# Performance work log

Measured on AMD Instinct MI355X. Metric: run time of the kernel, lower is better.

The kernel has to match this reference:

```python
import jax, jax.numpy as jnp
import numpy as np

N_NODES = 50000
N_EDGES = 800000
D_IN = 128
D_HID = 128
N_CLASSES = 40


def setup_inputs() -> dict:
    key = jax.random.key(0)
    ks = jax.random.split(key, 12)
    x = jax.random.normal(ks[0], (N_NODES, D_IN), dtype=jnp.float32)
    edge_index = jax.random.randint(ks[1], (2, N_EDGES), 0, N_NODES, dtype=jnp.int64)
    s1 = 1.0 / np.sqrt(D_IN)
    s2 = 1.0 / np.sqrt(D_HID)
    W1 = jax.random.uniform(ks[2], (D_IN, D_HID), jnp.float32, -s1, s1)
    b1 = jnp.zeros((D_HID,), jnp.float32)
    W2 = jax.random.uniform(ks[3], (D_HID, D_HID), jnp.float32, -s2, s2)
    b2 = jnp.zeros((D_HID,), jnp.float32)
    W3 = jax.random.uniform(ks[4], (D_HID, D_HID), jnp.float32, -s2, s2)
    b3 = jnp.zeros((D_HID,), jnp.float32)
    fcW = jax.random.uniform(ks[5], (D_HID, N_CLASSES), jnp.float32, -s2, s2)
    fcb = jax.random.uniform(ks[6], (N_CLASSES,), jnp.float32, -s2, s2)
    return {"x": x, "edge_index": edge_index, "W1": W1, "b1": b1,
            "W2": W2, "b2": b2, "W3": W3, "b3": b3, "fcW": fcW, "fcb": fcb}


def _gcn_norm(edge_index, n_nodes):
    # add self-loops, compute symmetric normalization deg^-1/2[src]*deg^-1/2[dst]
    loops = jnp.arange(n_nodes, dtype=edge_index.dtype)
    src = jnp.concatenate([edge_index[0], loops])
    dst = jnp.concatenate([edge_index[1], loops])
    deg = jax.ops.segment_sum(jnp.ones_like(dst, dtype=jnp.float32), dst,
                              num_segments=n_nodes)
    dinv = jax.lax.rsqrt(deg)  # deg >= 1 thanks to self-loops
    norm = dinv[src] * dinv[dst]  # [E+N]
    return src, dst, norm


def _gcn_conv(h, W, b, src, dst, norm, n_nodes):
    h = h @ W                               # [N, D]
    msg = h[src] * norm[:, None]            # [E+N, D] gather + scale
    out = jax.ops.segment_sum(msg, dst, num_segments=n_nodes)  # scatter-add
    return out + b


def reference(x, edge_index, W1, b1, W2, b2, W3, b3, fcW, fcb):
    n = x.shape[0]
    src, dst, norm = _gcn_norm(edge_index, n)
    h = jax.nn.relu(_gcn_conv(x, W1, b1, src, dst, norm, n))
    h = jax.nn.relu(_gcn_conv(h, W2, b2, src, dst, norm, n))
    h = jax.nn.relu(_gcn_conv(h, W3, b3, src, dst, norm, n))
    out = h @ fcW + fcb
    return (h, out)
```

## Files before the change

kernel.cpp:

```cpp
#include <hip/hip_runtime.h>
#include <hip/hip_fp16.h>

#define NN 50000
#define NE 800000
#define D  128
#define NC 40
#define NBLK ((NN + 255) / 256)
#define NXCD 8
#define DRANGE ((NN + NXCD - 1) / NXCD)
#define EPB 2048
#define NCH ((NE + EPB - 1) / EPB)
#define CAP 64
#define NTILE ((NN + 127) / 128)

typedef short bf16x8 __attribute__((ext_vector_type(8)));
typedef float f32x16 __attribute__((ext_vector_type(16)));

__device__ __forceinline__ void load_edge(const void* ei, int e, int is64, int& s, int& d) {
    if (is64) {
        const long long* p = (const long long*)ei;
        s = (int)p[e]; d = (int)p[NE + e];
    } else {
        const int* p = (const int*)ei;
        s = p[e]; d = p[NE + e];
    }
}

__global__ __launch_bounds__(256) void setup_kernel(int* __restrict__ cnt,
                                                    const int* __restrict__ ei,
                                                    int* __restrict__ flag) {
    if (blockIdx.x == NBLK) {
        __shared__ int nz;
        if (threadIdx.x == 0) nz = 0;
        __syncthreads();
        int c = 0;
        for (int i = threadIdx.x; i < 2048; i += 256)
            if (ei[2 * i + 1] != 0) c = 1;
        if (c) atomicAdd(&nz, 1);
        __syncthreads();
        if (threadIdx.x == 0) *flag = (nz == 0) ? 1 : 0;
    } else {
        int i = blockIdx.x * 256 + threadIdx.x;
        if (i < NN) cnt[i] = 0;
    }
}

__global__ __launch_bounds__(256) void fill_kernel(const void* ei, const int* __restrict__ flag,
                                                   int* cnt, int* __restrict__ srcs) {
    int r = blockIdx.x & (NXCD - 1);
    int chunk = blockIdx.x >> 3;
    int base = chunk * EPB;
    int dlo = r * DRANGE, dhi = dlo + DRANGE;
    int is64 = *flag;
#pragma unroll
    for (int j = 0; j < EPB / 256; ++j) {
        int e = base + threadIdx.x + j * 256;
        if (e >= NE) break;
        int s, d; load_edge(ei, e, is64, s, d);
        if (d < dlo || d >= dhi || (unsigned)d >= NN || (unsigned)s >= NN) continue;
        int slot = atomicAdd(&cnt[d], 1);
        if (slot < CAP) srcs[d * CAP + slot] = s;
    }
}

__global__ __launch_bounds__(256) void dinv_kernel(const int* __restrict__ cnt,
                                                   float* __restrict__ dinv) {
    int i = blockIdx.x * 256 + threadIdx.x;
    if (i < NN) dinv[i] = 1.0f / sqrtf((float)cnt[i] + 1.0f);
}

__global__ __launch_bounds__(256) void sort_kernel(const int* __restrict__ cnt,
                                                   int* __restrict__ srcs,
                                                   float* __restrict__ wts,
                                                   const float* __restrict__ dinv) {
    int wid = (blockIdx.x * 256 + threadIdx.x) >> 6;
    int lane = threadIdx.x & 63;
    if (wid >= NN) return;
    int deg = cnt[wid]; if (deg > CAP) deg = CAP;
    if (deg == 0) return;
    float di = dinv[wid];
    int base = wid * CAP;
    int v = (lane < deg) ? srcs[base + lane] : 0x7fffffff;
#pragma unroll
    for (int k = 2; k <= 64; k <<= 1) {
#pragma unroll
        for (int j = k >> 1; j > 0; j >>= 1) {
            int o = __shfl_xor(v, j);
            bool up = ((lane & k) == 0);
            bool lower = ((lane & j) == 0);
            int mn = min(v, o), mx = max(v, o);
            v = (lower == up) ? mn : mx;
        }
    }
    if (lane < deg) {
        srcs[base + lane] = v;
        wts[base + lane] = dinv[v] * di;
    }
}

__device__ __forceinline__ ushort f2bf(float x) {
    unsigned u = __float_as_uint(x);
    return (ushort)((u + 0x7fffu + ((u >> 16) & 1u)) >> 16);
}
__device__ __forceinline__ float bf2f(ushort h) {
    return __uint_as_float(((unsigned)h) << 16);
}

__global__ __launch_bounds__(128) void prep_all_kernel(const float* __restrict__ W1,
                                                       const float* __restrict__ W2,
                                                       const float* __restrict__ W3,
                                                       const float* __restrict__ fcW,
                                                       ushort* __restrict__ i1,
                                                       ushort* __restrict__ i2,
                                                       ushort* __restrict__ i3,
                                                       ushort* __restrict__ ifc) {
    int b = blockIdx.x;
    int k = threadIdx.x;
    if (b < 384) {
        const float* W = (b < 128) ? W1 : (b < 256) ? W2 : W3;
        ushort* img = (b < 128) ? i1 : (b < 256) ? i2 : i3;
        int c = b & 127;
        float w = W[(size_t)k * D + c];
        ushort hi = f2bf(w);
        ushort lo = f2bf(w - bf2f(hi));
        int ch = k >> 6, kk = k & 63, g = kk >> 3;
        int idx = c * 64 + ((g ^ (c & 7)) * 8) + (kk & 7);
        img[(size_t)(ch * 2 + 0) * 8192 + idx] = hi;
        img[(size_t)(ch * 2 + 1) * 8192 + idx] = lo;
    } else {
        int c = b - 384;
        float w = (c < NC) ? fcW[(size_t)k * NC + c] : 0.0f;
        ushort hi = f2bf(w);
        ushort lo = f2bf(w - bf2f(hi));
        int g = k >> 3;
        int idx = c * 128 + ((g ^ (c & 7)) * 8) + (k & 7);
        ifc[idx] = hi;
        ifc[8192 + idx] = lo;
    }
}

__global__ __launch_bounds__(256, 2) void gemm_f32_kernel(const float* __restrict__ A,
                                                          const ushort* __restrict__ Wimg,
                                                          ushort* __restrict__ T) {
    __shared__ alignas(16) ushort sAh[8192];
    __shared__ alignas(16) ushort sAl[8192];
    __shared__ alignas(16) ushort sWh[8192];
    __shared__ alignas(16) ushort sWl[8192];
    int tid = threadIdx.x;
    int wave = tid >> 6, lane = tid & 63;
    int wr = wave >> 1, wc = wave & 1;
    int m0 = blockIdx.x * 128;
    f32x16 acc[2][2];
#pragma unroll
    for (int i = 0; i < 2; ++i)
#pragma unroll
        for (int j = 0; j < 2; ++j)
#pragma unroll
            for (int q = 0; q < 16; ++q) acc[i][j][q] = 0.0f;

    for (int ch = 0; ch < 2; ++ch) {
        const float4* wh = (const float4*)(Wimg + (size_t)(ch * 2 + 0) * 8192);
        const float4* wl = (const float4*)(Wimg + (size_t)(ch * 2 + 1) * 8192);
#pragma unroll
        for (int i = 0; i < 4; ++i) {
            ((float4*)sWh)[tid + i * 256] = wh[tid + i * 256];
            ((float4*)sWl)[tid + i * 256] = wl[tid + i * 256];
        }
#pragma unroll
        for (int p = 0; p < 8; ++p) {
            int idx = tid + p * 256;
            int r = idx >> 4;
            int kq = idx & 15;
            float4 v = make_float4(0, 0, 0, 0);
            int grow = m0 + r;
            if (grow < NN) v = *(const float4*)(A + (size_t)grow * D + ch * 64 + kq * 4);
            ushort4 h, l;
            h.x = f2bf(v.x); l.x = f2bf(v.x - bf2f(h.x));
            h.y = f2bf(v.y); l.y = f2bf(v.y - bf2f(h.y));
            h.z = f2bf(v.z); l.z = f2bf(v.z - bf2f(h.z));
            h.w = f2bf(v.w); l.w = f2bf(v.w - bf2f(h.w));
            int g = kq >> 1, half = kq & 1;
            int uidx = r * 64 + ((g ^ (r & 7)) * 8) + half * 4;
            *(ushort4*)&sAh[uidx] = h;
            *(ushort4*)&sAl[uidx] = l;
        }
        __syncthreads();

        int rb = wr * 64 + (lane & 31);
        int cb = wc * 64 + (lane & 31);
#pragma unroll
        for (int s = 0; s < 4; ++s) {
            int gg = s * 2 + (lane >> 5);
            int ra0 = rb, ra1 = rb + 32;
            int ca0 = cb, ca1 = cb + 32;
            bf16x8 ah0 = *(const bf16x8*)&sAh[ra0 * 64 + ((gg ^ (ra0 & 7)) * 8)];
            bf16x8 ah1 = *(const bf16x8*)&sAh[ra1 * 64 + ((gg ^ (ra1 & 7)) * 8)];
            bf16x8 al0 = *(const bf16x8*)&sAl[ra0 * 64 + ((gg ^ (ra0 & 7)) * 8)];
            bf16x8 al1 = *(const bf16x8*)&sAl[ra1 * 64 + ((gg ^ (ra1 & 7)) * 8)];
            bf16x8 wh0 = *(const bf16x8*)&sWh[ca0 * 64 + ((gg ^ (ca0 & 7)) * 8)];
            bf16x8 wh1 = *(const bf16x8*)&sWh[ca1 * 64 + ((gg ^ (ca1 & 7)) * 8)];
            bf16x8 wl0 = *(const bf16x8*)&sWl[ca0 * 64 + ((gg ^ (ca0 & 7)) * 8)];
            bf16x8 wl1 = *(const bf16x8*)&sWl[ca1 * 64 + ((gg ^ (ca1 & 7)) * 8)];
            acc[0][0] = __builtin_amdgcn_mfma_f32_32x32x16_bf16(ah0, wh0, acc[0][0], 0, 0, 0);
            acc[0][0] = __builtin_amdgcn_mfma_f32_32x32x16_bf16(ah0, wl0, acc[0][0], 0, 0, 0);
            acc[0][0] = __builtin_amdgcn_mfma_f32_32x32x16_bf16(al0, wh0, acc[0][0], 0, 0, 0);
            acc[0][1] = __builtin_amdgcn_mfma_f32_32x32x16_bf16(ah0, wh1, acc[0][1], 0, 0, 0);
            acc[0][1] = __builtin_amdgcn_mfma_f32_32x32x16_bf16(ah0, wl1, acc[0][1], 0, 0, 0);
            acc[0][1] = __builtin_amdgcn_mfma_f32_32x32x16_bf16(al0, wh1, acc[0][1], 0, 0, 0);
            acc[1][0] = __builtin_amdgcn_mfma_f32_32x32x16_bf16(ah1, wh0, acc[1][0], 0, 0, 0);
            acc[1][0] = __builtin_amdgcn_mfma_f32_32x32x16_bf16(ah1, wl0, acc[1][0], 0, 0, 0);
            acc[1][0] = __builtin_amdgcn_mfma_f32_32x32x16_bf16(al1, wh0, acc[1][0], 0, 0, 0);
            acc[1][1] = __builtin_amdgcn_mfma_f32_32x32x16_bf16(ah1, wh1, acc[1][1], 0, 0, 0);
            acc[1][1] = __builtin_amdgcn_mfma_f32_32x32x16_bf16(ah1, wl1, acc[1][1], 0, 0, 0);
            acc[1][1] = __builtin_amdgcn_mfma_f32_32x32x16_bf16(al1, wh1, acc[1][1], 0, 0, 0);
        }
        __syncthreads();
    }
#pragma unroll
    for (int rt = 0; rt < 2; ++rt)
#pragma unroll
        for (int ct = 0; ct < 2; ++ct) {
            int cg = wc * 64 + ct * 32 + (lane & 31);
#pragma unroll
            for (int reg = 0; reg < 16; ++reg) {
                int row = m0 + wr * 64 + rt * 32 + (reg & 3) + 8 * (reg >> 2) + 4 * (lane >> 5);
                if (row < NN)
                    T[(size_t)row * D + cg] = __half_as_ushort(__float2half(acc[rt][ct][reg]));
            }
        }
}

__global__ __launch_bounds__(256, 2) void gemm_img_kernel(const ushort* __restrict__ Aimg,
                                                          const ushort* __restrict__ Wimg,
                                                          ushort* __restrict__ T) {
    __shared__ alignas(16) ushort sAh[8192];
    __shared__ alignas(16) ushort sAl[8192];
    __shared__ alignas(16) ushort sWh[8192];
    __shared__ alignas(16) ushort sWl[8192];
    int tid = threadIdx.x;
    int wave = tid >> 6, lane = tid & 63;
    int wr = wave >> 1, wc = wave & 1;
    int m0 = blockIdx.x * 128;
    const ushort* Atile = Aimg + (size_t)blockIdx.x * 32768;
    f32x16 acc[2][2];
#pragma unroll
    for (int i = 0; i < 2; ++i)
#pragma unroll
        for (int j = 0; j < 2; ++j)
#pragma unroll
            for (int q = 0; q < 16; ++q) acc[i][j][q] = 0.0f;

    for (int ch = 0; ch < 2; ++ch) {
        const float4* wh = (const float4*)(Wimg + (size_t)(ch * 2 + 0) * 8192);
        const float4* wl = (const float4*)(Wimg + (size_t)(ch * 2 + 1) * 8192);
        const float4* ah = (const float4*)(Atile + (size_t)(ch * 2 + 0) * 8192);
        const float4* al = (const float4*)(Atile + (size_t)(ch * 2 + 1) * 8192);
#pragma unroll
        for (int i = 0; i < 4; ++i) {
            ((float4*)sWh)[tid + i * 256] = wh[tid + i * 256];
            ((float4*)sWl)[tid + i * 256] = wl[tid + i * 256];
            ((float4*)sAh)[tid + i * 256] = ah[tid + i * 256];
            ((float4*)sAl)[tid + i * 256] = al[tid + i * 256];
        }
        __syncthreads();

        int rb = wr * 64 + (lane & 31);
        int cb = wc * 64 + (lane & 31);
#pragma unroll
        for (int s = 0; s < 4; ++s) {
            int gg = s * 2 + (lane >> 5);
            int ra0 = rb, ra1 = rb + 32;
            int ca0 = cb, ca1 = cb + 32;
            bf16x8 ah0 = *(const bf16x8*)&sAh[ra0 * 64 + ((gg ^ (ra0 & 7)) * 8)];
            bf16x8 ah1 = *(const bf16x8*)&sAh[ra1 * 64 + ((gg ^ (ra1 & 7)) * 8)];
            bf16x8 al0 = *(const bf16x8*)&sAl[ra0 * 64 + ((gg ^ (ra0 & 7)) * 8)];
            bf16x8 al1 = *(const bf16x8*)&sAl[ra1 * 64 + ((gg ^ (ra1 & 7)) * 8)];
            bf16x8 wh0 = *(const bf16x8*)&sWh[ca0 * 64 + ((gg ^ (ca0 & 7)) * 8)];
            bf16x8 wh1 = *(const bf16x8*)&sWh[ca1 * 64 + ((gg ^ (ca1 & 7)) * 8)];
            bf16x8 wl0 = *(const bf16x8*)&sWl[ca0 * 64 + ((gg ^ (ca0 & 7)) * 8)];
            bf16x8 wl1 = *(const bf16x8*)&sWl[ca1 * 64 + ((gg ^ (ca1 & 7)) * 8)];
            acc[0][0] = __builtin_amdgcn_mfma_f32_32x32x16_bf16(ah0, wh0, acc[0][0], 0, 0, 0);
            acc[0][0] = __builtin_amdgcn_mfma_f32_32x32x16_bf16(ah0, wl0, acc[0][0], 0, 0, 0);
            acc[0][0] = __builtin_amdgcn_mfma_f32_32x32x16_bf16(al0, wh0, acc[0][0], 0, 0, 0);
            acc[0][1] = __builtin_amdgcn_mfma_f32_32x32x16_bf16(ah0, wh1, acc[0][1], 0, 0, 0);
            acc[0][1] = __builtin_amdgcn_mfma_f32_32x32x16_bf16(ah0, wl1, acc[0][1], 0, 0, 0);
            acc[0][1] = __builtin_amdgcn_mfma_f32_32x32x16_bf16(al0, wh1, acc[0][1], 0, 0, 0);
            acc[1][0] = __builtin_amdgcn_mfma_f32_32x32x16_bf16(ah1, wh0, acc[1][0], 0, 0, 0);
            acc[1][0] = __builtin_amdgcn_mfma_f32_32x32x16_bf16(ah1, wl0, acc[1][0], 0, 0, 0);
            acc[1][0] = __builtin_amdgcn_mfma_f32_32x32x16_bf16(al1, wh0, acc[1][0], 0, 0, 0);
            acc[1][1] = __builtin_amdgcn_mfma_f32_32x32x16_bf16(ah1, wh1, acc[1][1], 0, 0, 0);
            acc[1][1] = __builtin_amdgcn_mfma_f32_32x32x16_bf16(ah1, wl1, acc[1][1], 0, 0, 0);
            acc[1][1] = __builtin_amdgcn_mfma_f32_32x32x16_bf16(al1, wh1, acc[1][1], 0, 0, 0);
        }
        __syncthreads();
    }
#pragma unroll
    for (int rt = 0; rt < 2; ++rt)
#pragma unroll
        for (int ct = 0; ct < 2; ++ct) {
            int cg = wc * 64 + ct * 32 + (lane & 31);
#pragma unroll
            for (int reg = 0; reg < 16; ++reg) {
                int row = m0 + wr * 64 + rt * 32 + (reg & 3) + 8 * (reg >> 2) + 4 * (lane >> 5);
                if (row < NN)
                    T[(size_t)row * D + cg] = __half_as_ushort(__float2half(acc[rt][ct][reg]));
            }
        }
}

__global__ __launch_bounds__(256, 2) void fc_mfma_kernel(const float* __restrict__ A,
                                                         const ushort* __restrict__ img,
                                                         const float* __restrict__ b,
                                                         float* __restrict__ O) {
    __shared__ alignas(16) ushort sAh[8192];
    __shared__ alignas(16) ushort sAl[8192];
    __shared__ alignas(16) ushort sWh[8192];
    __shared__ alignas(16) ushort sWl[8192];
    int tid = threadIdx.x;
    int wave = tid >> 6, lane = tid & 63;
    int m0 = blockIdx.x * 128;
#pragma unroll
    for (int i = 0; i < 4; ++i) {
        ((float4*)sWh)[tid + i * 256] = ((const float4*)img)[tid + i * 256];
        ((float4*)sWl)[tid + i * 256] = ((const float4*)(img + 8192))[tid + i * 256];
    }
    f32x16 acc[2];
#pragma unroll
    for (int j = 0; j < 2; ++j)
#pragma unroll
        for (int q = 0; q < 16; ++q) acc[j][q] = 0.0f;

    for (int ch = 0; ch < 2; ++ch) {
#pragma unroll
        for (int p = 0; p < 8; ++p) {
            int idx = tid + p * 256;
            int r = idx >> 4;
            int kq = idx & 15;
            float4 v = make_float4(0, 0, 0, 0);
            int grow = m0 + r;
            if (grow < NN) v = *(const float4*)(A + (size_t)grow * D + ch * 64 + kq * 4);
            ushort4 h, l;
            h.x = f2bf(v.x); l.x = f2bf(v.x - bf2f(h.x));
            h.y = f2bf(v.y); l.y = f2bf(v.y - bf2f(h.y));
            h.z = f2bf(v.z); l.z = f2bf(v.z - bf2f(h.z));
            h.w = f2bf(v.w); l.w = f2bf(v.w - bf2f(h.w));
            int g = kq >> 1, half = kq & 1;
            int uidx = r * 64 + ((g ^ (r & 7)) * 8) + half * 4;
            *(ushort4*)&sAh[uidx] = h;
            *(ushort4*)&sAl[uidx] = l;
        }
        __syncthreads();
        int ra = wave * 32 + (lane & 31);
        int c0 = lane & 31, c1 = 32 + (lane & 31);
#pragma unroll
        for (int s = 0; s < 4; ++s) {
            int gg = s * 2 + (lane >> 5);
            int kg = ch * 8 + gg;
            bf16x8 ah = *(const bf16x8*)&sAh[ra * 64 + ((gg ^ (ra & 7)) * 8)];
            bf16x8 al = *(const bf16x8*)&sAl[ra * 64 + ((gg ^ (ra & 7)) * 8)];
            bf16x8 wh0 = *(const bf16x8*)&sWh[c0 * 128 + ((kg ^ (c0 & 7)) * 8)];
            bf16x8 wl0 = *(const bf16x8*)&sWl[c0 * 128 + ((kg ^ (c0 & 7)) * 8)];
            bf16x8 wh1 = *(const bf16x8*)&sWh[c1 * 128 + ((kg ^ (c1 & 7)) * 8)];
            bf16x8 wl1 = *(const bf16x8*)&sWl[c1 * 128 + ((kg ^ (c1 & 7)) * 8)];
            acc[0] = __builtin_amdgcn_mfma_f32_32x32x16_bf16(ah, wh0, acc[0], 0, 0, 0);
            acc[0] = __builtin_amdgcn_mfma_f32_32x32x16_bf16(ah, wl0, acc[0], 0, 0, 0);
            acc[0] = __builtin_amdgcn_mfma_f32_32x32x16_bf16(al, wh0, acc[0], 0, 0, 0);
            acc[1] = __builtin_amdgcn_mfma_f32_32x32x16_bf16(ah, wh1, acc[1], 0, 0, 0);
            acc[1] = __builtin_amdgcn_mfma_f32_32x32x16_bf16(ah, wl1, acc[1], 0, 0, 0);
            acc[1] = __builtin_amdgcn_mfma_f32_32x32x16_bf16(al, wh1, acc[1], 0, 0, 0);
        }
        __syncthreads();
    }
#pragma unroll
    for (int ct = 0; ct < 2; ++ct) {
        int col = ct * 32 + (lane & 31);
        if (col < NC) {
            float bb = b[col];
#pragma unroll
            for (int reg = 0; reg < 16; ++reg) {
                int row = m0 + wave * 32 + (reg & 3) + 8 * (reg >> 2) + 4 * (lane >> 5);
                if (row < NN) O[(size_t)row * NC + col] = acc[ct][reg] + bb;
            }
        }
    }
}

__device__ __forceinline__ float4 h4load(const ushort* __restrict__ T, int row, int l) {
    uint2 hv = ((const uint2*)(T + (size_t)row * D))[l];
    __half2 h0 = *(__half2*)&hv.x, h1 = *(__half2*)&hv.y;
    float2 f0 = __half22float2(h0), f1 = __half22float2(h1);
    return make_float4(f0.x, f0.y, f1.x, f1.y);
}

__device__ __forceinline__ void fma4(float4& a, float4 v, float w) {
    a.x = fmaf(v.x, w, a.x); a.y = fmaf(v.y, w, a.y);
    a.z = fmaf(v.z, w, a.z); a.w = fmaf(v.w, w, a.w);
}

template<int IMG>
__global__ __launch_bounds__(256) void aggregate_kernel(const ushort* __restrict__ T,
                                                        const int* __restrict__ cnt,
                                                        const int* __restrict__ srcs,
                                                        const float* __restrict__ wts,
                                                        const float* __restrict__ dinv,
                                                        const float* __restrict__ b,
                                                        float* __restrict__ out,
                                                        ushort* __restrict__ img) {
    int wid = (blockIdx.x * 256 + threadIdx.x) >> 5;
    int l = threadIdx.x & 31;
    if (wid >= NN) return;
    float di = dinv[wid];
    float wself = di * di;
    float4 acc = h4load(T, wid, l);
    acc.x *= wself; acc.y *= wself; acc.z *= wself; acc.w *= wself;
    int base = wid * CAP;
    int deg = cnt[wid]; if (deg > CAP) deg = CAP;
    int e = 0;
    for (; e + 7 < deg; e += 8) {
        int s0 = srcs[base + e + 0], s1 = srcs[base + e + 1];
        int s2 = srcs[base + e + 2], s3 = srcs[base + e + 3];
        int s4 = srcs[base + e + 4], s5 = srcs[base + e + 5];
        int s6 = srcs[base + e + 6], s7 = srcs[base + e + 7];
        float4 v0 = h4load(T, s0, l), v1 = h4load(T, s1, l);
        float4 v2 = h4load(T, s2, l), v3 = h4load(T, s3, l);
        float4 v4 = h4load(T, s4, l), v5 = h4load(T, s5, l);
        float4 v6 = h4load(T, s6, l), v7 = h4load(T, s7, l);
        fma4(acc, v0, wts[base + e + 0]); fma4(acc, v1, wts[base + e + 1]);
        fma4(acc, v2, wts[base + e + 2]); fma4(acc, v3, wts[base + e + 3]);
        fma4(acc, v4, wts[base + e + 4]); fma4(acc, v5, wts[base + e + 5]);
        fma4(acc, v6, wts[base + e + 6]); fma4(acc, v7, wts[base + e + 7]);
    }
    for (; e + 3 < deg; e += 4) {
        int s0 = srcs[base + e + 0], s1 = srcs[base + e + 1];
        int s2 = srcs[base + e + 2], s3 = srcs[base + e + 3];
        float4 v0 = h4load(T, s0, l), v1 = h4load(T, s1, l);
        float4 v2 = h4load(T, s2, l), v3 = h4load(T, s3, l);
        fma4(acc, v0, wts[base + e + 0]); fma4(acc, v1, wts[base + e + 1]);
        fma4(acc, v2, wts[base + e + 2]); fma4(acc, v3, wts[base + e + 3]);
    }
    for (; e < deg; ++e) {
        fma4(acc, h4load(T, srcs[base + e], l), wts[base + e]);
    }
    float4 bb = ((const float4*)b)[l];
    acc.x = fmaxf(acc.x + bb.x, 0.0f);
    acc.y = fmaxf(acc.y + bb.y, 0.0f);
    acc.z = fmaxf(acc.z + bb.z, 0.0f);
    acc.w = fmaxf(acc.w + bb.w, 0.0f);
    if (IMG) {
        int tile = wid >> 7, rr = wid & 127;
        int c0 = 4 * l;
        int ch = c0 >> 6, kk = c0 & 63, g = kk >> 3;
        int idx = rr * 64 + ((g ^ (rr & 7)) * 8) + (kk & 7);
        ushort4 hh, ll;
        hh.x = f2bf(acc.x); ll.x = f2bf(acc.x - bf2f(hh.x));
        hh.y = f2bf(acc.y); ll.y = f2bf(acc.y - bf2f(hh.y));
        hh.z = f2bf(acc.z); ll.z = f2bf(acc.z - bf2f(hh.z));
        hh.w = f2bf(acc.w); ll.w = f2bf(acc.w - bf2f(hh.w));
        ushort* bimg = img + (size_t)tile * 32768;
        *(ushort4*)(bimg + (size_t)(ch * 2 + 0) * 8192 + idx) = hh;
        *(ushort4*)(bimg + (size_t)(ch * 2 + 1) * 8192 + idx) = ll;
    } else {
        ((float4*)(out + (size_t)wid * D))[l] = acc;
    }
}

extern "C" void kernel_launch(void* const* d_in, const int* in_sizes, int n_in,
                              void* d_out, int out_size, void* d_ws, size_t ws_size,
                              hipStream_t stream) {
    const float* x   = (const float*)d_in[0];
    const void*  ei  = d_in[1];
    const float* W1  = (const float*)d_in[2];
    const float* b1  = (const float*)d_in[3];
    const float* W2  = (const float*)d_in[4];
    const float* b2  = (const float*)d_in[5];
    const float* W3  = (const float*)d_in[6];
    const float* b3  = (const float*)d_in[7];
    const float* fcW = (const float*)d_in[8];
    const float* fcb = (const float*)d_in[9];

    float* out_h  = (float*)d_out;
    float* out_fc = out_h + (size_t)NN * D;

    size_t off = 0;
    auto alloc = [&](size_t bytes) {
        void* p = (char*)d_ws + off;
        off += (bytes + 255) & ~(size_t)255;
        return p;
    };
    float*  dinv   = (float*) alloc((size_t)NN * 4);
    int*    cnt    = (int*)   alloc((size_t)NN * 4);
    int*    flag   = (int*)   alloc(256);
    int*    srcs   = (int*)   alloc((size_t)NN * CAP * 4);
    float*  wts    = (float*) alloc((size_t)NN * CAP * 4);
    ushort* bufT   = (ushort*)alloc((size_t)NN * D * 2);
    ushort* himg   = (ushort*)alloc((size_t)NTILE * 32768 * 2);
    ushort* wimg1  = (ushort*)alloc(32768 * 2);
    ushort* wimg2  = (ushort*)alloc(32768 * 2);
    ushort* wimg3  = (ushort*)alloc(32768 * 2);
    ushort* fcimg  = (ushort*)alloc(16384 * 2);
    (void)ws_size; (void)in_sizes; (void)n_in; (void)out_size;

    setup_kernel<<<NBLK + 1, 256, 0, stream>>>(cnt, (const int*)ei, flag);
    prep_all_kernel<<<448, 128, 0, stream>>>(W1, W2, W3, fcW, wimg1, wimg2, wimg3, fcimg);
    fill_kernel<<<NCH * NXCD, 256, 0, stream>>>(ei, flag, cnt, srcs);
    dinv_kernel<<<NBLK, 256, 0, stream>>>(cnt, dinv);
    sort_kernel<<<(NN * 64 + 255) / 256, 256, 0, stream>>>(cnt, srcs, wts, dinv);

    int agg_grid = (NN * 32 + 255) / 256;
    gemm_f32_kernel<<<NTILE, 256, 0, stream>>>(x, wimg1, bufT);
    aggregate_kernel<1><<<agg_grid, 256, 0, stream>>>(bufT, cnt, srcs, wts, dinv, b1, nullptr, himg);
    gemm_img_kernel<<<NTILE, 256, 0, stream>>>(himg, wimg2, bufT);
    aggregate_kernel<1><<<agg_grid, 256, 0, stream>>>(bufT, cnt, srcs, wts, dinv, b2, nullptr, himg);
    gemm_img_kernel<<<NTILE, 256, 0, stream>>>(himg, wimg3, bufT);
    aggregate_kernel<0><<<agg_grid, 256, 0, stream>>>(bufT, cnt, srcs, wts, dinv, b3, out_h, nullptr);

    fc_mfma_kernel<<<NTILE, 256, 0, stream>>>(out_h, fcimg, fcb, out_fc);
}
```

Baseline: 219.9 us.

## Merge setup and weight prep kernels, batch edge loads, shuffle-broadcast neighbor lists

```diff
diff --git a/kernel.cpp b/kernel.cpp
--- a/kernel.cpp
+++ b/kernel.cpp
@@ -6,6 +6,7 @@
 #define D  128
 #define NC 40
 #define NBLK ((NN + 255) / 256)
+#define NB128 ((NN + 127) / 128)
 #define NXCD 8
 #define DRANGE ((NN + NXCD - 1) / NXCD)
 #define EPB 2048
@@ -26,22 +27,63 @@
     }
 }
 
-__global__ __launch_bounds__(256) void setup_kernel(int* __restrict__ cnt,
-                                                    const int* __restrict__ ei,
-                                                    int* __restrict__ flag) {
-    if (blockIdx.x == NBLK) {
+__device__ __forceinline__ ushort f2bf(float x) {
+    unsigned u = __float_as_uint(x);
+    return (ushort)((u + 0x7fffu + ((u >> 16) & 1u)) >> 16);
+}
+__device__ __forceinline__ float bf2f(ushort h) {
+    return __uint_as_float(((unsigned)h) << 16);
+}
+
+__global__ __launch_bounds__(128) void setup_prep_kernel(int* __restrict__ cnt,
+                                                         const int* __restrict__ ei,
+                                                         int* __restrict__ flag,
+                                                         const float* __restrict__ W1,
+                                                         const float* __restrict__ W2,
+                                                         const float* __restrict__ W3,
+                                                         const float* __restrict__ fcW,
+                                                         ushort* __restrict__ i1,
+                                                         ushort* __restrict__ i2,
+                                                         ushort* __restrict__ i3,
+                                                         ushort* __restrict__ ifc) {
+    int b = blockIdx.x;
+    int k = threadIdx.x;
+    if (b < NB128) {
+        int i = b * 128 + k;
+        if (i < NN) cnt[i] = 0;
+    } else if (b == NB128) {
         __shared__ int nz;
-        if (threadIdx.x == 0) nz = 0;
+        if (k == 0) nz = 0;
         __syncthreads();
         int c = 0;
-        for (int i = threadIdx.x; i < 2048; i += 256)
+        for (int i = k; i < 2048; i += 128)
             if (ei[2 * i + 1] != 0) c = 1;
         if (c) atomicAdd(&nz, 1);
         __syncthreads();
-        if (threadIdx.x == 0) *flag = (nz == 0) ? 1 : 0;
+        if (k == 0) *flag = (nz == 0) ? 1 : 0;
     } else {
-        int i = blockIdx.x * 256 + threadIdx.x;
-        if (i < NN) cnt[i] = 0;
+        int bb = b - (NB128 + 1);
+        if (bb < 384) {
+            const float* W = (bb < 128) ? W1 : (bb < 256) ? W2 : W3;
+            ushort* img = (bb < 128) ? i1 : (bb < 256) ? i2 : i3;
+            int c = bb & 127;
+            float w = W[(size_t)k * D + c];
+            ushort hi = f2bf(w);
+            ushort lo = f2bf(w - bf2f(hi));
+            int ch = k >> 6, kk = k & 63, g = kk >> 3;
+            int idx = c * 64 + ((g ^ (c & 7)) * 8) + (kk & 7);
+            img[(size_t)(ch * 2 + 0) * 8192 + idx] = hi;
+            img[(size_t)(ch * 2 + 1) * 8192 + idx] = lo;
+        } else {
+            int c = bb - 384;
+            float w = (c < NC) ? fcW[(size_t)k * NC + c] : 0.0f;
+            ushort hi = f2bf(w);
+            ushort lo = f2bf(w - bf2f(hi));
+            int g = k >> 3;
+            int idx = c * 128 + ((g ^ (c & 7)) * 8) + (k & 7);
+            ifc[idx] = hi;
+            ifc[8192 + idx] = lo;
+        }
     }
 }
 
@@ -49,17 +91,22 @@
                                                    int* cnt, int* __restrict__ srcs) {
     int r = blockIdx.x & (NXCD - 1);
     int chunk = blockIdx.x >> 3;
-    int base = chunk * EPB;
+    int base = chunk * EPB + threadIdx.x * 8;
     int dlo = r * DRANGE, dhi = dlo + DRANGE;
     int is64 = *flag;
-#pragma unroll
-    for (int j = 0; j < EPB / 256; ++j) {
-        int e = base + threadIdx.x + j * 256;
-        if (e >= NE) break;
-        int s, d; load_edge(ei, e, is64, s, d);
-        if (d < dlo || d >= dhi || (unsigned)d >= NN || (unsigned)s >= NN) continue;
-        int slot = atomicAdd(&cnt[d], 1);
-        if (slot < CAP) srcs[d * CAP + slot] = s;
+    int s[8], d[8];
+#pragma unroll
+    for (int j = 0; j < 8; ++j) {
+        int e = base + j;
+        if (e < NE) load_edge(ei, e, is64, s[j], d[j]);
+        else { s[j] = -1; d[j] = -1; }
+    }
+#pragma unroll
+    for (int j = 0; j < 8; ++j) {
+        int dd = d[j];
+        if (dd < dlo || dd >= dhi || (unsigned)dd >= NN || (unsigned)s[j] >= NN) continue;
+        int slot = atomicAdd(&cnt[dd], 1);
+        if (slot < CAP) srcs[dd * CAP + slot] = s[j];
     }
 }
 
@@ -95,47 +142,6 @@
     if (lane < deg) {
         srcs[base + lane] = v;
         wts[base + lane] = dinv[v] * di;
-    }
-}
-
-__device__ __forceinline__ ushort f2bf(float x) {
-    unsigned u = __float_as_uint(x);
-    return (ushort)((u + 0x7fffu + ((u >> 16) & 1u)) >> 16);
-}
-__device__ __forceinline__ float bf2f(ushort h) {
-    return __uint_as_float(((unsigned)h) << 16);
-}
-
-__global__ __launch_bounds__(128) void prep_all_kernel(const float* __restrict__ W1,
-                                                       const float* __restrict__ W2,
-                                                       const float* __restrict__ W3,
-                                                       const float* __restrict__ fcW,
-                                                       ushort* __restrict__ i1,
-                                                       ushort* __restrict__ i2,
-                                                       ushort* __restrict__ i3,
-                                                       ushort* __restrict__ ifc) {
-    int b = blockIdx.x;
-    int k = threadIdx.x;
-    if (b < 384) {
-        const float* W = (b < 128) ? W1 : (b < 256) ? W2 : W3;
-        ushort* img = (b < 128) ? i1 : (b < 256) ? i2 : i3;
-        int c = b & 127;
-        float w = W[(size_t)k * D + c];
-        ushort hi = f2bf(w);
-        ushort lo = f2bf(w - bf2f(hi));
-        int ch = k >> 6, kk = k & 63, g = kk >> 3;
-        int idx = c * 64 + ((g ^ (c & 7)) * 8) + (kk & 7);
-        img[(size_t)(ch * 2 + 0) * 8192 + idx] = hi;
-        img[(size_t)(ch * 2 + 1) * 8192 + idx] = lo;
-    } else {
-        int c = b - 384;
-        float w = (c < NC) ? fcW[(size_t)k * NC + c] : 0.0f;
-        ushort hi = f2bf(w);
-        ushort lo = f2bf(w - bf2f(hi));
-        int g = k >> 3;
-        int idx = c * 128 + ((g ^ (c & 7)) * 8) + (k & 7);
-        ifc[idx] = hi;
-        ifc[8192 + idx] = lo;
     }
 }
 
@@ -415,28 +421,34 @@
     acc.x *= wself; acc.y *= wself; acc.z *= wself; acc.w *= wself;
     int base = wid * CAP;
     int deg = cnt[wid]; if (deg > CAP) deg = CAP;
+    int lim = deg < 32 ? deg : 32;
+    int sreg = 0; float wreg = 0.0f;
+    if (l < lim) { sreg = srcs[base + l]; wreg = wts[base + l]; }
     int e = 0;
-    for (; e + 7 < deg; e += 8) {
-        int s0 = srcs[base + e + 0], s1 = srcs[base + e + 1];
-        int s2 = srcs[base + e + 2], s3 = srcs[base + e + 3];
-        int s4 = srcs[base + e + 4], s5 = srcs[base + e + 5];
-        int s6 = srcs[base + e + 6], s7 = srcs[base + e + 7];
+    for (; e + 7 < lim; e += 8) {
+        int s0 = __shfl(sreg, e + 0, 32), s1 = __shfl(sreg, e + 1, 32);
+        int s2 = __shfl(sreg, e + 2, 32), s3 = __shfl(sreg, e + 3, 32);
+        int s4 = __shfl(sreg, e + 4, 32), s5 = __shfl(sreg, e + 5, 32);
+        int s6 = __shfl(sreg, e + 6, 32), s7 = __shfl(sreg, e + 7, 32);
         float4 v0 = h4load(T, s0, l), v1 = h4load(T, s1, l);
         float4 v2 = h4load(T, s2, l), v3 = h4load(T, s3, l);
         float4 v4 = h4load(T, s4, l), v5 = h4load(T, s5, l);
         float4 v6 = h4load(T, s6, l), v7 = h4load(T, s7, l);
-        fma4(acc, v0, wts[base + e + 0]); fma4(acc, v1, wts[base + e + 1]);
-        fma4(acc, v2, wts[base + e + 2]); fma4(acc, v3, wts[base + e + 3]);
-        fma4(acc, v4, wts[base + e + 4]); fma4(acc, v5, wts[base + e + 5]);
-        fma4(acc, v6, wts[base + e + 6]); fma4(acc, v7, wts[base + e + 7]);
-    }
-    for (; e + 3 < deg; e += 4) {
-        int s0 = srcs[base + e + 0], s1 = srcs[base + e + 1];
-        int s2 = srcs[base + e + 2], s3 = srcs[base + e + 3];
+        fma4(acc, v0, __shfl(wreg, e + 0, 32)); fma4(acc, v1, __shfl(wreg, e + 1, 32));
+        fma4(acc, v2, __shfl(wreg, e + 2, 32)); fma4(acc, v3, __shfl(wreg, e + 3, 32));
+        fma4(acc, v4, __shfl(wreg, e + 4, 32)); fma4(acc, v5, __shfl(wreg, e + 5, 32));
+        fma4(acc, v6, __shfl(wreg, e + 6, 32)); fma4(acc, v7, __shfl(wreg, e + 7, 32));
+    }
+    for (; e + 3 < lim; e += 4) {
+        int s0 = __shfl(sreg, e + 0, 32), s1 = __shfl(sreg, e + 1, 32);
+        int s2 = __shfl(sreg, e + 2, 32), s3 = __shfl(sreg, e + 3, 32);
         float4 v0 = h4load(T, s0, l), v1 = h4load(T, s1, l);
         float4 v2 = h4load(T, s2, l), v3 = h4load(T, s3, l);
-        fma4(acc, v0, wts[base + e + 0]); fma4(acc, v1, wts[base + e + 1]);
-        fma4(acc, v2, wts[base + e + 2]); fma4(acc, v3, wts[base + e + 3]);
+        fma4(acc, v0, __shfl(wreg, e + 0, 32)); fma4(acc, v1, __shfl(wreg, e + 1, 32));
+        fma4(acc, v2, __shfl(wreg, e + 2, 32)); fma4(acc, v3, __shfl(wreg, e + 3, 32));
+    }
+    for (; e < lim; ++e) {
+        fma4(acc, h4load(T, __shfl(sreg, e, 32), l), __shfl(wreg, e, 32));
     }
     for (; e < deg; ++e) {
         fma4(acc, h4load(T, srcs[base + e], l), wts[base + e]);
@@ -500,8 +512,9 @@
     ushort* fcimg  = (ushort*)alloc(16384 * 2);
     (void)ws_size; (void)in_sizes; (void)n_in; (void)out_size;
 
-    setup_kernel<<<NBLK + 1, 256, 0, stream>>>(cnt, (const int*)ei, flag);
-    prep_all_kernel<<<448, 128, 0, stream>>>(W1, W2, W3, fcW, wimg1, wimg2, wimg3, fcimg);
+    setup_prep_kernel<<<NB128 + 1 + 448, 128, 0, stream>>>(cnt, (const int*)ei, flag,
+                                                           W1, W2, W3, fcW,
+                                                           wimg1, wimg2, wimg3, fcimg);
     fill_kernel<<<NCH * NXCD, 256, 0, stream>>>(ei, flag, cnt, srcs);
     dinv_kernel<<<NBLK, 256, 0, stream>>>(cnt, dinv);
     sort_kernel<<<(NN * 64 + 255) / 256, 256, 0, stream>>>(cnt, srcs, wts, dinv);
```

New measurement: 217.1 us. No clear change (-1.3%).
